# Kernel optimization log

Measured on AMD Instinct MI355X. Metric: run time of the kernel, lower is better.

## Reference

```python
import jax, jax.numpy as jnp
import numpy as np

ROUTING_ITERS = 3
EPS = 1e-12


def squash(s):
    # squash over both pose-matrix dims (axis=[-2,-1])
    n2 = jnp.sum(s * s, axis=(-2, -1), keepdims=True)
    n = jnp.sqrt(n2 + EPS)
    return s * (n2 / (1.0 + n2)) / n


def setup_inputs() -> dict:
    key = jax.random.key(0)
    k1, k2, k3 = jax.random.split(key, 3)
    B, I, O = 32, 4096, 32
    input_poses = jax.random.normal(k1, (B, I, 4, 4), dtype=jnp.float32)
    input_activations = jax.random.uniform(k2, (B, I), dtype=jnp.float32)
    # weight: [num_capsules, num_input_caps, 4, 4] (trans_in=trans_out=False for 4x4->4x4)
    w = jax.random.normal(k3, (O, I, 4, 4), dtype=jnp.float32) * 0.05
    return {"input_poses": input_poses, "input_activations": input_activations, "w": w}


def reference(input_poses, input_activations, w):
    # votes: expand_dims(poses,1) @ w, broadcast over output capsules -> [B,O,I,4,4]
    votes = jnp.einsum("bixy,oiyz->boixz", input_poses, w)
    B, O, I = votes.shape[0], votes.shape[1], votes.shape[2]

    # dynamic routing (routing-by-agreement)
    b = jnp.zeros((B, O, I), dtype=votes.dtype)
    s = None
    for it in range(ROUTING_ITERS):
        c = jax.nn.softmax(b, axis=1)  # couple over output capsules
        s = jnp.einsum("boi,boixy->boxy", c, votes)  # weighted sum [B,O,4,4]
        if it < ROUTING_ITERS - 1:
            v = squash(s)
            b = b + jnp.einsum("boixy,boxy->boi", votes, v)

    capsule_poses = squash(s)  # activation == 'squash'
    capsule_activations = jnp.sqrt(jnp.sum(capsule_poses * capsule_poses, axis=(-2, -1)) + EPS)
    return capsule_poses, capsule_activations
```

## Files before the change

### kernel.cpp

```cpp
#include <hip/hip_runtime.h>
#include <math.h>


#define NB 32
#define NI 4096
#define NO 32
#define I_TILE 16
#define NCHUNK (NI / I_TILE)
#define B_TILE 8
#define NBG (NB / B_TILE)
#define SOFF (NB * NO * 16)
#define EPSF 1e-12f

#define W_OSTR 10
#define W_ISTR (32 * W_OSTR)
#define W_WORDS (I_TILE * W_ISTR)
#define P_WORDS (B_TILE * I_TILE * 8)

typedef _Float16 v2h __attribute__((ext_vector_type(2)));

#if __has_builtin(__builtin_amdgcn_fdot2)
__device__ __forceinline__ float fdot2(v2h a, v2h b, float c) {
    return __builtin_amdgcn_fdot2(a, b, c, false);
}
#else
__device__ __forceinline__ float fdot2(v2h a, v2h b, float c) {
    return fmaf((float)a.x, (float)b.x, fmaf((float)a.y, (float)b.y, c));
}
#endif

#if __has_builtin(__builtin_amdgcn_cvt_pkrtz)
__device__ __forceinline__ v2h pk2h(float a, float b) {
    return __builtin_bit_cast(v2h, __builtin_amdgcn_cvt_pkrtz(a, b));
}
#else
__device__ __forceinline__ v2h pk2h(float a, float b) {
    v2h r; r.x = (_Float16)a; r.y = (_Float16)b; return r;
}
#endif

__device__ __forceinline__ v2h bch(unsigned u) {
    return __builtin_bit_cast(v2h, u);
}

__device__ __forceinline__ float dot4(const float4 a, const float4 b) {
    return fmaf(a.x, b.x, fmaf(a.y, b.y, fmaf(a.z, b.z, a.w * b.w)));
}

__device__ __forceinline__ void fma4(float4& s, const float c, const float4 t) {
    s.x = fmaf(c, t.x, s.x);
    s.y = fmaf(c, t.y, s.y);
    s.z = fmaf(c, t.z, s.z);
    s.w = fmaf(c, t.w, s.w);
}

__device__ __forceinline__ void add4(float4& s, const float4 t) {
    s.x += t.x; s.y += t.y; s.z += t.z; s.w += t.w;
}

template <int CTRL>
__device__ __forceinline__ float dpp_add(float x) {
    int xi = __builtin_bit_cast(int, x);
    int yi = __builtin_amdgcn_update_dpp(0, xi, CTRL, 0xf, 0xf, false);
    return x + __builtin_bit_cast(float, yi);
}

__device__ __forceinline__ float sum32(float x) {
    x = dpp_add<0xB1>(x);
    x = dpp_add<0x4E>(x);
    x = dpp_add<0x141>(x);
    x = dpp_add<0x140>(x);
#if __has_builtin(__builtin_amdgcn_permlane16_swap)
    typedef unsigned uv2 __attribute__((ext_vector_type(2)));
    const unsigned xi = __builtin_bit_cast(unsigned, x);
    uv2 r = __builtin_amdgcn_permlane16_swap(xi, xi, false, false);
    return __builtin_bit_cast(float, r.x) + __builtin_bit_cast(float, r.y);
#else
    int t = __builtin_amdgcn_ds_swizzle(__builtin_bit_cast(int, x), 0x401F);
    return x + __builtin_bit_cast(float, t);
#endif
}

__global__ __launch_bounds__(256, 4) void caps_pass_h(
    const float* __restrict__ poses, const float* __restrict__ w,
    const float* __restrict__ v_buf, float* __restrict__ s_part,
    const int pass)
{
    __shared__ unsigned wsw[W_WORDS];
    __shared__ unsigned psw[P_WORDS];
    const int tid    = threadIdx.x;
    const int chunk  = blockIdx.x;
    const int bgroup = blockIdx.y;
    const int ibase  = chunk * I_TILE;

    #pragma unroll
    for (int r = 0; r < 4; ++r) {
        const int idx = r * 256 + tid;
        const int o_l = idx >> 5;
        const int l   = idx & 31;
        const int i_l = l >> 1;
        const int m   = l & 1;
        const float* g = w + (((size_t)o_l * NI + ibase + i_l) << 4) + (m << 3);
        const float4 A = *(const float4*)g;
        const float4 B = *(const float4*)(g + 4);
        const v2h c0 = pk2h(A.x, B.x), c1 = pk2h(A.y, B.y);
        const v2h c2 = pk2h(A.z, B.z), c3 = pk2h(A.w, B.w);
        const int base = i_l * W_ISTR + o_l * W_OSTR + (m << 2);
        *(uint2*)&wsw[base]     = make_uint2(__builtin_bit_cast(unsigned, c0),
                                             __builtin_bit_cast(unsigned, c1));
        *(uint2*)&wsw[base + 2] = make_uint2(__builtin_bit_cast(unsigned, c2),
                                             __builtin_bit_cast(unsigned, c3));
    }
    #pragma unroll
    for (int r = 0; r < 2; ++r) {
        const int idx = r * 256 + tid;
        const int b_l = idx >> 6;
        const int l   = idx & 63;
        const int i_l = l >> 2;
        const int x   = l & 3;
        const float4 row = *(const float4*)(
            poses + (((size_t)(bgroup * B_TILE + b_l) * NI + ibase + i_l) << 4)
                  + (x << 2));
        const v2h c0 = pk2h(row.x, row.y), c1 = pk2h(row.z, row.w);
        *(uint2*)&psw[((b_l * I_TILE + i_l) << 3) + (x << 1)] =
            make_uint2(__builtin_bit_cast(unsigned, c0),
                       __builtin_bit_cast(unsigned, c1));
    }

    const int o    = tid & 31;
    const int bsub = tid >> 5;
    const int b    = bgroup * B_TILE + bsub;
    const int bo   = b * NO + o;

    float4 vv0 = {0,0,0,0}, vv1 = {0,0,0,0}, vv2 = {0,0,0,0}, vv3 = {0,0,0,0};
    if (pass > 0) {
        const float4* vp = (const float4*)(v_buf + (bo << 4));
        vv0 = vp[0]; vv1 = vp[1]; vv2 = vp[2]; vv3 = vp[3];
    }

    const unsigned* wrow = &wsw[o * W_OSTR];
    const unsigned* prow = &psw[(bsub * I_TILE) << 3];

    __syncthreads();

    float4 s0 = {0,0,0,0}, s1 = {0,0,0,0}, s2 = {0,0,0,0}, s3 = {0,0,0,0};

    #pragma unroll 2
    for (int i = 0; i < I_TILE; ++i) {
        const uint2 wa = *(const uint2*)&wrow[i * W_ISTR + 0];
        const uint2 wb = *(const uint2*)&wrow[i * W_ISTR + 2];
        const uint2 wc = *(const uint2*)&wrow[i * W_ISTR + 4];
        const uint2 wd = *(const uint2*)&wrow[i * W_ISTR + 6];
        const uint4 pa = *(const uint4*)&prow[(i << 3) + 0];
        const uint4 pb = *(const uint4*)&prow[(i << 3) + 4];

        const v2h p00 = bch(pa.x), p01 = bch(pa.y);
        const v2h p10 = bch(pa.z), p11 = bch(pa.w);
        const v2h p20 = bch(pb.x), p21 = bch(pb.y);
        const v2h p30 = bch(pb.z), p31 = bch(pb.w);
        const v2h w00 = bch(wa.x), w01 = bch(wa.y);
        const v2h w02 = bch(wb.x), w03 = bch(wb.y);
        const v2h w10 = bch(wc.x), w11 = bch(wc.y);
        const v2h w12 = bch(wd.x), w13 = bch(wd.y);

        float4 t0, t1, t2, t3;
        t0.x = fdot2(p00, w00, fdot2(p01, w10, 0.0f));
        t0.y = fdot2(p00, w01, fdot2(p01, w11, 0.0f));
        t0.z = fdot2(p00, w02, fdot2(p01, w12, 0.0f));
        t0.w = fdot2(p00, w03, fdot2(p01, w13, 0.0f));
        t1.x = fdot2(p10, w00, fdot2(p11, w10, 0.0f));
        t1.y = fdot2(p10, w01, fdot2(p11, w11, 0.0f));
        t1.z = fdot2(p10, w02, fdot2(p11, w12, 0.0f));
        t1.w = fdot2(p10, w03, fdot2(p11, w13, 0.0f));
        t2.x = fdot2(p20, w00, fdot2(p21, w10, 0.0f));
        t2.y = fdot2(p20, w01, fdot2(p21, w11, 0.0f));
        t2.z = fdot2(p20, w02, fdot2(p21, w12, 0.0f));
        t2.w = fdot2(p20, w03, fdot2(p21, w13, 0.0f));
        t3.x = fdot2(p30, w00, fdot2(p31, w10, 0.0f));
        t3.y = fdot2(p30, w01, fdot2(p31, w11, 0.0f));
        t3.z = fdot2(p30, w02, fdot2(p31, w12, 0.0f));
        t3.w = fdot2(p30, w03, fdot2(p31, w13, 0.0f));

        float cc;
        if (pass == 0) {
            cc = 1.0f / 32.0f;
        } else {
            const float d = dot4(t0,vv0) + dot4(t1,vv1)
                          + dot4(t2,vv2) + dot4(t3,vv3);
            const float e  = __expf(d);
            const float es = sum32(e);
            cc = __fdividef(e, es);
        }
        fma4(s0, cc, t0); fma4(s1, cc, t1);
        fma4(s2, cc, t2); fma4(s3, cc, t3);
    }

    float4* sp = (float4*)(s_part + ((size_t)chunk * (NB * NO) + bo) * 16);
    sp[0] = s0; sp[1] = s1; sp[2] = s2; sp[3] = s3;
}

__global__ __launch_bounds__(256) void caps_reduce4(
    const float* __restrict__ s_part, float* __restrict__ v_buf,
    float* __restrict__ out, const int pass)
{
    const int e   = threadIdx.x & 15;
    const int grp = threadIdx.x >> 4;
    const int v4g = blockIdx.x * 16 + e;

    const float4* sp4 = (const float4*)s_part;
    float4 acc = {0, 0, 0, 0};
    #pragma unroll
    for (int j = 0; j < NCHUNK / 16; ++j) {
        const int c = grp + (j << 4);
        add4(acc, sp4[(size_t)c * (SOFF / 4) + v4g]);
    }

    __shared__ float4 red4[16][17];
    red4[grp][e] = acc;
    __syncthreads();

    if (threadIdx.x < 16) {
        float4 a = red4[0][e];
        #pragma unroll
        for (int g = 1; g < 16; ++g) add4(a, red4[g][e]);
        float x = dot4(a, a);
        x += __shfl_xor(x, 1, 4);
        x += __shfl_xor(x, 2, 4);
        const float n2 = x;
        const float n  = sqrtf(n2 + EPSF);
        const float sc = (n2 / (1.0f + n2)) / n;
        if (pass < 2) {
            float4* vp = (float4*)v_buf + v4g;
            float4 vold = {0, 0, 0, 0};
            if (pass > 0) vold = *vp;
            *vp = make_float4(fmaf(sc, a.x, vold.x), fmaf(sc, a.y, vold.y),
                              fmaf(sc, a.z, vold.z), fmaf(sc, a.w, vold.w));
        } else {
            ((float4*)out)[v4g] =
                make_float4(sc * a.x, sc * a.y, sc * a.z, sc * a.w);
            if ((e & 3) == 0)
                out[NB * NO * 16 + (v4g >> 2)] = sqrtf(n2 * sc * sc + EPSF);
        }
    }
}

#define FB_CHUNKS 32
#define FB_IPB (NI / FB_CHUNKS)

__device__ __forceinline__ float4 row_mm(const float4 p, const float4 w0,
                                         const float4 w1, const float4 w2,
                                         const float4 w3) {
    float4 r;
    r.x = fmaf(p.x, w0.x, fmaf(p.y, w1.x, fmaf(p.z, w2.x, p.w * w3.x)));
    r.y = fmaf(p.x, w0.y, fmaf(p.y, w1.y, fmaf(p.z, w2.y, p.w * w3.y)));
    r.z = fmaf(p.x, w0.z, fmaf(p.y, w1.z, fmaf(p.z, w2.z, p.w * w3.z)));
    r.w = fmaf(p.x, w0.w, fmaf(p.y, w1.w, fmaf(p.z, w2.w, p.w * w3.w)));
    return r;
}

__global__ __launch_bounds__(256) void caps_pass_fb(
    const float* __restrict__ poses, const float* __restrict__ w,
    const float* __restrict__ v_buf, float* __restrict__ s_buf, const int mode)
{
    const int tid   = threadIdx.x;
    const int b     = blockIdx.y;
    const int chunk = blockIdx.x;
    const int o     = tid & 31;
    const int g     = tid >> 5;

    float4 v0 = {0,0,0,0}, v1 = {0,0,0,0}, v2 = {0,0,0,0}, v3 = {0,0,0,0};
    if (mode != 0) {
        const float4* vp = (const float4*)(v_buf + (((b * NO) + o) << 4));
        v0 = vp[0]; v1 = vp[1]; v2 = vp[2]; v3 = vp[3];
    }
    float4 s0 = {0,0,0,0}, s1 = {0,0,0,0}, s2 = {0,0,0,0}, s3 = {0,0,0,0};
    const int ibase = chunk * FB_IPB + g;
    #pragma unroll 4
    for (int it = 0; it < FB_IPB / 8; ++it) {
        const int i = ibase + (it << 3);
        const float4* ppf = (const float4*)(poses + ((((size_t)b * NI) + i) << 4));
        const float4 p0 = ppf[0], p1 = ppf[1], p2 = ppf[2], p3 = ppf[3];
        const float4* wpf = (const float4*)(w + ((((size_t)o * NI) + i) << 4));
        const float4 w0 = wpf[0], w1 = wpf[1], w2 = wpf[2], w3 = wpf[3];
        const float4 t0 = row_mm(p0, w0, w1, w2, w3);
        const float4 t1 = row_mm(p1, w0, w1, w2, w3);
        const float4 t2 = row_mm(p2, w0, w1, w2, w3);
        const float4 t3 = row_mm(p3, w0, w1, w2, w3);
        float cc;
        if (mode == 0) {
            cc = 1.0f / 32.0f;
        } else {
            float d = dot4(t0,v0) + dot4(t1,v1) + dot4(t2,v2) + dot4(t3,v3);
            const float e  = __expf(d);
            const float es = sum32(e);
            cc = __fdividef(e, es);
        }
        fma4(s0, cc, t0); fma4(s1, cc, t1);
        fma4(s2, cc, t2); fma4(s3, cc, t3);
    }
    __shared__ float red[8][32][16];
    float4* rp = (float4*)&red[g][o][0];
    rp[0] = s0; rp[1] = s1; rp[2] = s2; rp[3] = s3;
    __syncthreads();
    for (int idx = tid; idx < NO * 16; idx += 256) {
        const int oo = idx >> 4;
        const int k  = idx & 15;
        float acc = red[0][oo][k];
        #pragma unroll
        for (int gg = 1; gg < 8; ++gg) acc += red[gg][oo][k];
        atomicAdd(&s_buf[(((b * NO) + oo) << 4) + k], acc);
    }
}

__global__ __launch_bounds__(256) void caps_squash_fb(
    float* __restrict__ s_buf, float* __restrict__ v_buf,
    float* __restrict__ out, const int mode)
{
    const int idx = blockIdx.x * 256 + threadIdx.x;
    if (idx >= NB * NO) return;
    float4* sp = (float4*)(s_buf + (idx << 4));
    const float4 s0 = sp[0], s1 = sp[1], s2 = sp[2], s3 = sp[3];
    const float n2 = dot4(s0,s0) + dot4(s1,s1) + dot4(s2,s2) + dot4(s3,s3);
    const float n  = sqrtf(n2 + EPSF);
    const float sc = (n2 / (1.0f + n2)) / n;
    if (mode == 2) {
        float4* op = (float4*)(out + (idx << 4));
        op[0] = make_float4(sc*s0.x, sc*s0.y, sc*s0.z, sc*s0.w);
        op[1] = make_float4(sc*s1.x, sc*s1.y, sc*s1.z, sc*s1.w);
        op[2] = make_float4(sc*s2.x, sc*s2.y, sc*s2.z, sc*s2.w);
        op[3] = make_float4(sc*s3.x, sc*s3.y, sc*s3.z, sc*s3.w);
        out[NB * NO * 16 + idx] = sqrtf(n2 * sc * sc + EPSF);
    } else {
        float4* vp = (float4*)(v_buf + (idx << 4));
        float4 a0 = {0,0,0,0}, a1 = {0,0,0,0}, a2 = {0,0,0,0}, a3 = {0,0,0,0};
        if (mode != 0) { a0 = vp[0]; a1 = vp[1]; a2 = vp[2]; a3 = vp[3]; }
        vp[0] = make_float4(fmaf(sc,s0.x,a0.x), fmaf(sc,s0.y,a0.y), fmaf(sc,s0.z,a0.z), fmaf(sc,s0.w,a0.w));
        vp[1] = make_float4(fmaf(sc,s1.x,a1.x), fmaf(sc,s1.y,a1.y), fmaf(sc,s1.z,a1.z), fmaf(sc,s1.w,a1.w));
        vp[2] = make_float4(fmaf(sc,s2.x,a2.x), fmaf(sc,s2.y,a2.y), fmaf(sc,s2.z,a2.z), fmaf(sc,s2.w,a2.w));
        vp[3] = make_float4(fmaf(sc,s3.x,a3.x), fmaf(sc,s3.y,a3.y), fmaf(sc,s3.z,a3.z), fmaf(sc,s3.w,a3.w));
        const float4 z = {0,0,0,0};
        sp[0] = z; sp[1] = z; sp[2] = z; sp[3] = z;
    }
}

extern "C" void kernel_launch(void* const* d_in, const int* in_sizes, int n_in,
                              void* d_out, int out_size, void* d_ws, size_t ws_size,
                              hipStream_t stream) {
    (void)in_sizes; (void)n_in; (void)out_size;
    const float* poses = (const float*)d_in[0];
    const float* w     = (const float*)d_in[2];
    float* out = (float*)d_out;

    const size_t need = ((size_t)NCHUNK * SOFF + SOFF) * sizeof(float);
    if (ws_size >= need) {
        float* s_part = (float*)d_ws;
        float* v_buf  = s_part + (size_t)NCHUNK * SOFF;
        dim3 gp(NCHUNK, NBG), blk(256), gr(256);
        for (int pass = 0; pass < 3; ++pass) {
            caps_pass_h<<<gp, blk, 0, stream>>>(poses, w, v_buf, s_part, pass);
            caps_reduce4<<<gr, blk, 0, stream>>>(s_part, v_buf, out, pass);
        }
    } else {
        float* s_buf = (float*)d_ws;
        float* v_buf = s_buf + SOFF;
        (void)hipMemsetAsync(s_buf, 0, SOFF * sizeof(float), stream);
        dim3 grid(FB_CHUNKS, NB), block(256);
        for (int pass = 0; pass < 3; ++pass) {
            caps_pass_fb<<<grid, block, 0, stream>>>(poses, w, v_buf, s_buf, pass);
            caps_squash_fb<<<4, 256, 0, stream>>>(s_buf, v_buf, out, pass);
        }
    }
}
```

Measured before the change: 128.9 us.

## Cache fp16-packed weight/pose tiles in workspace and double batch tile per block

Pass 0 now writes the fp16-packed, LDS-layout weight and pose tiles out to workspace images, and passes 1 and 2 copy those images straight into shared memory instead of re-reading fp32 inputs and re-converting them. B_TILE doubles to 16, so each thread handles two batch rows and reuses the weight fragments loaded from LDS. This halves the number of blocks that load each weight tile. It aims to cut global read bytes and conversion work in the later passes. In exchange it adds global writes in pass 0, uses more workspace, and drops the occupancy hint from 4 to 2 blocks because of higher register use.

```diff
diff --git a/kernel.cpp b/kernel.cpp
--- a/kernel.cpp
+++ b/kernel.cpp
@@ -7,7 +7,7 @@
 #define NO 32
 #define I_TILE 16
 #define NCHUNK (NI / I_TILE)
-#define B_TILE 8
+#define B_TILE 16
 #define NBG (NB / B_TILE)
 #define SOFF (NB * NO * 16)
 #define EPSF 1e-12f
@@ -81,9 +81,10 @@
 #endif
 }
 
-__global__ __launch_bounds__(256, 4) void caps_pass_h(
+__global__ __launch_bounds__(256, 2) void caps_pass_h(
     const float* __restrict__ poses, const float* __restrict__ w,
     const float* __restrict__ v_buf, float* __restrict__ s_part,
+    unsigned* __restrict__ w_img, unsigned* __restrict__ p_img,
     const int pass)
 {
     __shared__ unsigned wsw[W_WORDS];
@@ -93,57 +94,93 @@
     const int bgroup = blockIdx.y;
     const int ibase  = chunk * I_TILE;
 
-    #pragma unroll
-    for (int r = 0; r < 4; ++r) {
-        const int idx = r * 256 + tid;
-        const int o_l = idx >> 5;
-        const int l   = idx & 31;
-        const int i_l = l >> 1;
-        const int m   = l & 1;
-        const float* g = w + (((size_t)o_l * NI + ibase + i_l) << 4) + (m << 3);
-        const float4 A = *(const float4*)g;
-        const float4 B = *(const float4*)(g + 4);
-        const v2h c0 = pk2h(A.x, B.x), c1 = pk2h(A.y, B.y);
-        const v2h c2 = pk2h(A.z, B.z), c3 = pk2h(A.w, B.w);
-        const int base = i_l * W_ISTR + o_l * W_OSTR + (m << 2);
-        *(uint2*)&wsw[base]     = make_uint2(__builtin_bit_cast(unsigned, c0),
-                                             __builtin_bit_cast(unsigned, c1));
-        *(uint2*)&wsw[base + 2] = make_uint2(__builtin_bit_cast(unsigned, c2),
-                                             __builtin_bit_cast(unsigned, c3));
-    }
-    #pragma unroll
-    for (int r = 0; r < 2; ++r) {
-        const int idx = r * 256 + tid;
-        const int b_l = idx >> 6;
-        const int l   = idx & 63;
-        const int i_l = l >> 2;
-        const int x   = l & 3;
-        const float4 row = *(const float4*)(
-            poses + (((size_t)(bgroup * B_TILE + b_l) * NI + ibase + i_l) << 4)
-                  + (x << 2));
-        const v2h c0 = pk2h(row.x, row.y), c1 = pk2h(row.z, row.w);
-        *(uint2*)&psw[((b_l * I_TILE + i_l) << 3) + (x << 1)] =
-            make_uint2(__builtin_bit_cast(unsigned, c0),
-                       __builtin_bit_cast(unsigned, c1));
+    if (pass == 0) {
+        #pragma unroll
+        for (int r = 0; r < 4; ++r) {
+            const int idx = r * 256 + tid;
+            const int o_l = idx >> 5;
+            const int l   = idx & 31;
+            const int i_l = l >> 1;
+            const int m   = l & 1;
+            const float* g = w + (((size_t)o_l * NI + ibase + i_l) << 4) + (m << 3);
+            const float4 A = *(const float4*)g;
+            const float4 B = *(const float4*)(g + 4);
+            const v2h c0 = pk2h(A.x, B.x), c1 = pk2h(A.y, B.y);
+            const v2h c2 = pk2h(A.z, B.z), c3 = pk2h(A.w, B.w);
+            const int base = i_l * W_ISTR + o_l * W_OSTR + (m << 2);
+            *(uint2*)&wsw[base]     = make_uint2(__builtin_bit_cast(unsigned, c0),
+                                                 __builtin_bit_cast(unsigned, c1));
+            *(uint2*)&wsw[base + 2] = make_uint2(__builtin_bit_cast(unsigned, c2),
+                                                 __builtin_bit_cast(unsigned, c3));
+        }
+        #pragma unroll
+        for (int r = 0; r < 4; ++r) {
+            const int idx = r * 256 + tid;
+            const int b_l = idx >> 6;
+            const int l   = idx & 63;
+            const int i_l = l >> 2;
+            const int x   = l & 3;
+            const float4 row = *(const float4*)(
+                poses + (((size_t)(bgroup * B_TILE + b_l) * NI + ibase + i_l) << 4)
+                      + (x << 2));
+            const v2h c0 = pk2h(row.x, row.y), c1 = pk2h(row.z, row.w);
+            *(uint2*)&psw[((b_l * I_TILE + i_l) << 3) + (x << 1)] =
+                make_uint2(__builtin_bit_cast(unsigned, c0),
+                           __builtin_bit_cast(unsigned, c1));
+        }
+    } else {
+        #pragma unroll
+        for (int r = 0; r < 5; ++r) {
+            const int j = (r * 256 + tid) << 2;
+            *(uint4*)&wsw[j] = *(const uint4*)&w_img[(size_t)chunk * W_WORDS + j];
+        }
+        #pragma unroll
+        for (int r = 0; r < 2; ++r) {
+            const int j = (r * 256 + tid) << 2;
+            *(uint4*)&psw[j] =
+                *(const uint4*)&p_img[((size_t)bgroup * NCHUNK + chunk) * P_WORDS + j];
+        }
     }
 
     const int o    = tid & 31;
     const int bsub = tid >> 5;
-    const int b    = bgroup * B_TILE + bsub;
-    const int bo   = b * NO + o;
-
-    float4 vv0 = {0,0,0,0}, vv1 = {0,0,0,0}, vv2 = {0,0,0,0}, vv3 = {0,0,0,0};
+    const int b0l  = bsub << 1;
+    const int b0   = bgroup * B_TILE + b0l;
+
+    float4 vv[2][4] = {{{0,0,0,0},{0,0,0,0},{0,0,0,0},{0,0,0,0}},
+                       {{0,0,0,0},{0,0,0,0},{0,0,0,0},{0,0,0,0}}};
     if (pass > 0) {
-        const float4* vp = (const float4*)(v_buf + (bo << 4));
-        vv0 = vp[0]; vv1 = vp[1]; vv2 = vp[2]; vv3 = vp[3];
-    }
-
-    const unsigned* wrow = &wsw[o * W_OSTR];
-    const unsigned* prow = &psw[(bsub * I_TILE) << 3];
+        #pragma unroll
+        for (int h = 0; h < 2; ++h) {
+            const float4* vp = (const float4*)(v_buf + (((b0 + h) * NO + o) << 4));
+            vv[h][0] = vp[0]; vv[h][1] = vp[1]; vv[h][2] = vp[2]; vv[h][3] = vp[3];
+        }
+    }
+
+    const unsigned* wrow  = &wsw[o * W_OSTR];
+    const unsigned* prow0 = &psw[(b0l * I_TILE) << 3];
+    const unsigned* prow1 = &psw[((b0l + 1) * I_TILE) << 3];
 
     __syncthreads();
 
-    float4 s0 = {0,0,0,0}, s1 = {0,0,0,0}, s2 = {0,0,0,0}, s3 = {0,0,0,0};
+    if (pass == 0) {
+        if (bgroup == 0) {
+            #pragma unroll
+            for (int r = 0; r < 5; ++r) {
+                const int j = (r * 256 + tid) << 2;
+                *(uint4*)&w_img[(size_t)chunk * W_WORDS + j] = *(const uint4*)&wsw[j];
+            }
+        }
+        #pragma unroll
+        for (int r = 0; r < 2; ++r) {
+            const int j = (r * 256 + tid) << 2;
+            *(uint4*)&p_img[((size_t)bgroup * NCHUNK + chunk) * P_WORDS + j] =
+                *(const uint4*)&psw[j];
+        }
+    }
+
+    float4 s[2][4] = {{{0,0,0,0},{0,0,0,0},{0,0,0,0},{0,0,0,0}},
+                      {{0,0,0,0},{0,0,0,0},{0,0,0,0},{0,0,0,0}}};
 
     #pragma unroll 2
     for (int i = 0; i < I_TILE; ++i) {
@@ -151,52 +188,61 @@
         const uint2 wb = *(const uint2*)&wrow[i * W_ISTR + 2];
         const uint2 wc = *(const uint2*)&wrow[i * W_ISTR + 4];
         const uint2 wd = *(const uint2*)&wrow[i * W_ISTR + 6];
-        const uint4 pa = *(const uint4*)&prow[(i << 3) + 0];
-        const uint4 pb = *(const uint4*)&prow[(i << 3) + 4];
-
-        const v2h p00 = bch(pa.x), p01 = bch(pa.y);
-        const v2h p10 = bch(pa.z), p11 = bch(pa.w);
-        const v2h p20 = bch(pb.x), p21 = bch(pb.y);
-        const v2h p30 = bch(pb.z), p31 = bch(pb.w);
         const v2h w00 = bch(wa.x), w01 = bch(wa.y);
         const v2h w02 = bch(wb.x), w03 = bch(wb.y);
         const v2h w10 = bch(wc.x), w11 = bch(wc.y);
         const v2h w12 = bch(wd.x), w13 = bch(wd.y);
 
-        float4 t0, t1, t2, t3;
-        t0.x = fdot2(p00, w00, fdot2(p01, w10, 0.0f));
-        t0.y = fdot2(p00, w01, fdot2(p01, w11, 0.0f));
-        t0.z = fdot2(p00, w02, fdot2(p01, w12, 0.0f));
-        t0.w = fdot2(p00, w03, fdot2(p01, w13, 0.0f));
-        t1.x = fdot2(p10, w00, fdot2(p11, w10, 0.0f));
-        t1.y = fdot2(p10, w01, fdot2(p11, w11, 0.0f));
-        t1.z = fdot2(p10, w02, fdot2(p11, w12, 0.0f));
-        t1.w = fdot2(p10, w03, fdot2(p11, w13, 0.0f));
-        t2.x = fdot2(p20, w00, fdot2(p21, w10, 0.0f));
-        t2.y = fdot2(p20, w01, fdot2(p21, w11, 0.0f));
-        t2.z = fdot2(p20, w02, fdot2(p21, w12, 0.0f));
-        t2.w = fdot2(p20, w03, fdot2(p21, w13, 0.0f));
-        t3.x = fdot2(p30, w00, fdot2(p31, w10, 0.0f));
-        t3.y = fdot2(p30, w01, fdot2(p31, w11, 0.0f));
-        t3.z = fdot2(p30, w02, fdot2(p31, w12, 0.0f));
-        t3.w = fdot2(p30, w03, fdot2(p31, w13, 0.0f));
-
-        float cc;
-        if (pass == 0) {
-            cc = 1.0f / 32.0f;
-        } else {
-            const float d = dot4(t0,vv0) + dot4(t1,vv1)
-                          + dot4(t2,vv2) + dot4(t3,vv3);
-            const float e  = __expf(d);
-            const float es = sum32(e);
-            cc = __fdividef(e, es);
-        }
-        fma4(s0, cc, t0); fma4(s1, cc, t1);
-        fma4(s2, cc, t2); fma4(s3, cc, t3);
-    }
-
-    float4* sp = (float4*)(s_part + ((size_t)chunk * (NB * NO) + bo) * 16);
-    sp[0] = s0; sp[1] = s1; sp[2] = s2; sp[3] = s3;
+        #pragma unroll
+        for (int h = 0; h < 2; ++h) {
+            const unsigned* pr = h ? prow1 : prow0;
+            const uint4 pa = *(const uint4*)&pr[(i << 3) + 0];
+            const uint4 pb = *(const uint4*)&pr[(i << 3) + 4];
+
+            const v2h p00 = bch(pa.x), p01 = bch(pa.y);
+            const v2h p10 = bch(pa.z), p11 = bch(pa.w);
+            const v2h p20 = bch(pb.x), p21 = bch(pb.y);
+            const v2h p30 = bch(pb.z), p31 = bch(pb.w);
+
+            float4 t0, t1, t2, t3;
+            t0.x = fdot2(p00, w00, fdot2(p01, w10, 0.0f));
+            t0.y = fdot2(p00, w01, fdot2(p01, w11, 0.0f));
+            t0.z = fdot2(p00, w02, fdot2(p01, w12, 0.0f));
+            t0.w = fdot2(p00, w03, fdot2(p01, w13, 0.0f));
+            t1.x = fdot2(p10, w00, fdot2(p11, w10, 0.0f));
+            t1.y = fdot2(p10, w01, fdot2(p11, w11, 0.0f));
+            t1.z = fdot2(p10, w02, fdot2(p11, w12, 0.0f));
+            t1.w = fdot2(p10, w03, fdot2(p11, w13, 0.0f));
+            t2.x = fdot2(p20, w00, fdot2(p21, w10, 0.0f));
+            t2.y = fdot2(p20, w01, fdot2(p21, w11, 0.0f));
+            t2.z = fdot2(p20, w02, fdot2(p21, w12, 0.0f));
+            t2.w = fdot2(p20, w03, fdot2(p21, w13, 0.0f));
+            t3.x = fdot2(p30, w00, fdot2(p31, w10, 0.0f));
+            t3.y = fdot2(p30, w01, fdot2(p31, w11, 0.0f));
+            t3.z = fdot2(p30, w02, fdot2(p31, w12, 0.0f));
+            t3.w = fdot2(p30, w03, fdot2(p31, w13, 0.0f));
+
+            float cc;
+            if (pass == 0) {
+                cc = 1.0f / 32.0f;
+            } else {
+                const float d = dot4(t0, vv[h][0]) + dot4(t1, vv[h][1])
+                              + dot4(t2, vv[h][2]) + dot4(t3, vv[h][3]);
+                const float e  = __expf(d);
+                const float es = sum32(e);
+                cc = __fdividef(e, es);
+            }
+            fma4(s[h][0], cc, t0); fma4(s[h][1], cc, t1);
+            fma4(s[h][2], cc, t2); fma4(s[h][3], cc, t3);
+        }
+    }
+
+    #pragma unroll
+    for (int h = 0; h < 2; ++h) {
+        const int bo = (b0 + h) * NO + o;
+        float4* sp = (float4*)(s_part + ((size_t)chunk * (NB * NO) + bo) * 16);
+        sp[0] = s[h][0]; sp[1] = s[h][1]; sp[2] = s[h][2]; sp[3] = s[h][3];
+    }
 }
 
 __global__ __launch_bounds__(256) void caps_reduce4(
@@ -351,13 +397,19 @@
     const float* w     = (const float*)d_in[2];
     float* out = (float*)d_out;
 
-    const size_t need = ((size_t)NCHUNK * SOFF + SOFF) * sizeof(float);
+    const size_t n_spart = (size_t)NCHUNK * SOFF;
+    const size_t n_wimg  = (size_t)NCHUNK * W_WORDS;
+    const size_t n_pimg  = (size_t)NBG * NCHUNK * P_WORDS;
+    const size_t need = (n_spart + SOFF + n_wimg + n_pimg) * 4;
     if (ws_size >= need) {
-        float* s_part = (float*)d_ws;
-        float* v_buf  = s_part + (size_t)NCHUNK * SOFF;
+        float*    s_part = (float*)d_ws;
+        float*    v_buf  = s_part + n_spart;
+        unsigned* w_img  = (unsigned*)(v_buf + SOFF);
+        unsigned* p_img  = w_img + n_wimg;
         dim3 gp(NCHUNK, NBG), blk(256), gr(256);
         for (int pass = 0; pass < 3; ++pass) {
-            caps_pass_h<<<gp, blk, 0, stream>>>(poses, w, v_buf, s_part, pass);
+            caps_pass_h<<<gp, blk, 0, stream>>>(poses, w, v_buf, s_part,
+                                                w_img, p_img, pass);
             caps_reduce4<<<gr, blk, 0, stream>>>(s_part, v_buf, out, pass);
         }
     } else {
```

Measured after the change: 136.0 us. +5.5%, slower.
